# Kernel tuning notes

Measured on AMD Instinct MI355X. Metric: run time of the kernel, lower is better.

## Reference

```python
import jax, jax.numpy as jnp
import numpy as np
from jax import lax

INPLANES = 512
PLANES = 512
MID = PLANES // 4  # expansion = 4
G = 4              # patch_groups
EPS = 1e-5


def _conv(x, w, groups, pad):
    return lax.conv_general_dilated(
        x, w, window_strides=(1, 1), padding=[(pad, pad), (pad, pad)],
        dimension_numbers=('NCHW', 'OIHW', 'NCHW'), feature_group_count=groups)


def _bn(x, gamma, beta, mean, var):
    scale = gamma / jnp.sqrt(var + EPS)
    return x * scale[None, :, None, None] + (beta - mean * scale)[None, :, None, None]


def _upmask(mask, c, h, w):
    # [b,g,mh,mw] -> repeat each group over c//g channels (group-major channel order),
    # then nearest-upsample to (h, w) (exact integer repeat, matches F.interpolate nearest)
    b, g, mh, mw = mask.shape
    m = jnp.repeat(mask, c // g, axis=1)
    m = jnp.repeat(m, h // mh, axis=2)
    m = jnp.repeat(m, w // mw, axis=3)
    return m


def setup_inputs() -> dict:
    key = jax.random.key(0)
    ks = jax.random.split(key, 20)
    x = jax.random.normal(ks[0], (16, INPLANES, 56, 56), dtype=jnp.float32)
    mask = jax.random.randint(ks[1], (16, G, 7, 7), 0, 2).astype(jnp.float32)
    s = 0.05
    w1 = jax.random.normal(ks[2], (MID, INPLANES // G, 1, 1), dtype=jnp.float32) * s
    w2 = jax.random.normal(ks[3], (MID, MID // G, 3, 3), dtype=jnp.float32) * s
    w3 = jax.random.normal(ks[4], (PLANES, MID // G, 1, 1), dtype=jnp.float32) * s
    def bnp(k, c):
        k1, k2, k3, k4 = jax.random.split(k, 4)
        return (jax.random.normal(k1, (c,), jnp.float32) * 0.1 + 1.0,  # gamma
                jax.random.normal(k2, (c,), jnp.float32) * 0.1,        # beta
                jax.random.normal(k3, (c,), jnp.float32) * 0.1,        # running mean
                jax.random.uniform(k4, (c,), jnp.float32, 0.5, 1.5))   # running var
    g1, b1, m1, v1 = bnp(ks[5], MID)
    g2, b2, m2, v2 = bnp(ks[6], MID)
    g3, b3, m3, v3 = bnp(ks[7], PLANES)
    return dict(x=x, mask=mask, w1=w1, g1=g1, b1=b1, m1=m1, v1=v1,
                w2=w2, g2=g2, b2=b2, m2=m2, v2=v2,
                w3=w3, g3=g3, b3=b3, m3=m3, v3=v3)


def reference(x, mask, w1, g1, b1, m1, v1, w2, g2, b2, m2, v2, w3, g3, b3, m3, v3):
    b, c, h, w = x.shape
    residual = x
    mask1 = _upmask(mask, c, h, w)           # [b, c, h, w]
    out = x * mask1
    out = jax.nn.relu(_bn(_conv(out, w1, G, 0), g1, b1, m1, v1))  # [b, MID, h, w]
    mask2 = _upmask(mask, out.shape[1], h, w)
    out = out * mask2
    out = jax.nn.relu(_bn(_conv(out, w2, G, 1), g2, b2, m2, v2))
    out = out * mask2
    out = _bn(_conv(out, w3, G, 0), g3, b3, m3, v3)
    out = out + residual
    return jax.nn.relu(out)
```

## Files before the change

### kernel.cpp

```cpp
#include <hip/hip_runtime.h>
#include <stdint.h>

typedef unsigned short U16;
typedef unsigned int   U32;
typedef __attribute__((ext_vector_type(8))) short short8;
typedef __attribute__((ext_vector_type(4))) float floatx4;

#define HW 3136

__device__ __forceinline__ U16 f2b(float f){
    union { float f; unsigned int i; } v; v.f = f;
    unsigned int u = (v.i + 0x7FFFu + ((v.i >> 16) & 1u)) >> 16;
    return (U16)u;
}
__device__ __forceinline__ short8 pack8(const float* p){
    float4 a = *reinterpret_cast<const float4*>(p);
    float4 b = *reinterpret_cast<const float4*>(p + 4);
    short8 r;
    r[0]=(short)f2b(a.x); r[1]=(short)f2b(a.y); r[2]=(short)f2b(a.z); r[3]=(short)f2b(a.w);
    r[4]=(short)f2b(b.x); r[5]=(short)f2b(b.y); r[6]=(short)f2b(b.z); r[7]=(short)f2b(b.w);
    return r;
}

__global__ void k_pre(const float* __restrict__ w2,
                      const float* g1, const float* b1, const float* m1, const float* v1,
                      const float* g2, const float* b2, const float* m2, const float* v2,
                      const float* g3, const float* b3, const float* m3, const float* v3,
                      U16* __restrict__ w2t, float* __restrict__ bn){
  int i = blockIdx.x * 256 + threadIdx.x;
  if (i < 4*9*32*32) {
    int ic  = i & 31;
    int oc  = (i >> 5) & 31;
    int gt  = i >> 10;
    int g_  = gt / 9, tap = gt % 9;
    w2t[i] = f2b(w2[((g_*32 + oc)*32 + ic)*9 + tap]);
  } else {
    int j = i - 4*9*32*32;
    if (j >= 768) return;
    const float *gp, *bp, *mp, *vp; int c, so, sho;
    if (j < 128)      { c = j;       gp=g1; bp=b1; mp=m1; vp=v1; so = 0;   sho = 128;  }
    else if (j < 256) { c = j - 128; gp=g2; bp=b2; mp=m2; vp=v2; so = 256; sho = 384;  }
    else              { c = j - 256; gp=g3; bp=b3; mp=m3; vp=v3; so = 512; sho = 1024; }
    float s = gp[c] / sqrtf(vp[c] + 1e-5f);
    bn[so + c]  = s;
    bn[sho + c] = bp[c] - mp[c] * s;
  }
}

__global__ __launch_bounds__(512) void k_conv1(const float* __restrict__ x,
        const float* __restrict__ mask, const float* __restrict__ w1,
        const float* __restrict__ bn, U16* __restrict__ t1){
  const int t = threadIdx.x;
  const int lane = t & 63, wave = t >> 6;
  const int quad = lane >> 4, l15 = lane & 15;
  const int oct = wave & 1, pxq = wave >> 1;
  const int b = blockIdx.z, g = blockIdx.y, mh = blockIdx.x;
  const int h0 = mh*8, wbase = pxq*112;
  __shared__ float mk[7];
  __shared__ __align__(16) U16 xs[32*456];
  if (t < 7) mk[t] = mask[((b*4 + g)*7 + mh)*7 + t];
  const float* xg = x + (size_t)(b*512 + g*128)*HW + h0*56;
  U16* t1g = t1 + (size_t)(b*128 + g*32)*HW + h0*56;

  const float* wg = w1 + (size_t)(g*32)*128;
  short8 afr[4];
  #pragma unroll
  for (int ks = 0; ks < 4; ++ks)
    afr[ks] = pack8(wg + (oct*16 + l15)*128 + ks*32 + quad*8);

  floatx4 acc[7] = {};
  #pragma unroll
  for (int ch = 0; ch < 4; ++ch){
    __syncthreads();
    #pragma unroll
    for (int k = 0; k < 7; ++k){
      int idx = k*512 + t;
      int ic = idx / 112, f = idx - ic*112;
      int px = f*4;
      float4 v = *reinterpret_cast<const float4*>(xg + (size_t)(ch*32 + ic)*HW + px);
      float m = mk[(px % 56) >> 3];
      U32 lo = (U32)f2b(v.x*m) | ((U32)f2b(v.y*m) << 16);
      U32 hi = (U32)f2b(v.z*m) | ((U32)f2b(v.w*m) << 16);
      *reinterpret_cast<uint2*>(&xs[ic*456 + px]) = make_uint2(lo, hi);
    }
    __syncthreads();
    #pragma unroll
    for (int pxt = 0; pxt < 7; ++pxt){
      short8 bfr;
      #pragma unroll
      for (int j = 0; j < 8; ++j)
        bfr[j] = (short)xs[(quad*8 + j)*456 + wbase + pxt*16 + l15];
      acc[pxt] = __builtin_amdgcn_mfma_f32_16x16x32_bf16(afr[ch], bfr, acc[pxt], 0,0,0);
    }
  }
  #pragma unroll
  for (int reg = 0; reg < 4; ++reg){
    int oc = oct*16 + quad*4 + reg;
    float sc = bn[g*32 + oc], sh = bn[128 + g*32 + oc];
    #pragma unroll
    for (int pxt = 0; pxt < 7; ++pxt){
      int px = wbase + pxt*16 + l15;
      float y = fmaxf(sc*acc[pxt][reg] + sh, 0.0f) * mk[(px % 56) >> 3];
      t1g[(size_t)oc*HW + px] = f2b(y);
    }
  }
}

__global__ __launch_bounds__(512) void k_conv2(const U16* __restrict__ t1,
        const float* __restrict__ mask, const U16* __restrict__ w2t,
        const float* __restrict__ bn, U16* __restrict__ t2){
  const int t = threadIdx.x;
  const int lane = t & 63, wave = t >> 6;
  const int quad = lane >> 4, l15 = lane & 15;
  const int oct = wave & 1, rq = wave >> 1;
  const int b = blockIdx.z, g = blockIdx.y, mh = blockIdx.x;
  const int h0 = mh*8;
  __shared__ float mk[7];
  __shared__ __align__(16) U16 s[32*720];
  if (t < 7) mk[t] = mask[((b*4 + g)*7 + mh)*7 + t];
  if (t < 320){
    int ic = t / 10, r = t - ic*10;
    s[(ic*10 + r)*72 + 7]  = 0;
    s[(ic*10 + r)*72 + 64] = 0;
  }
  const U16* tg = t1 + (size_t)(b*128 + g*32)*HW;
  #pragma unroll
  for (int k = 0; k < 5; ++k){
    int idx = k*512 + t;
    if (idx < 2240){
      int ic = idx / 70, rem = idx - ic*70;
      int r = rem / 7, seg = rem - r*7;
      int hh = h0 - 1 + r;
      uint4 v = make_uint4(0,0,0,0);
      if (hh >= 0 && hh < 56)
        v = *reinterpret_cast<const uint4*>(tg + (size_t)ic*HW + hh*56 + seg*8);
      *reinterpret_cast<uint4*>(&s[(ic*10 + r)*72 + 8 + seg*8]) = v;
    }
  }
  __syncthreads();
  const U16* wg = w2t + g*9*32*32;
  floatx4 acc[7] = {};
  #pragma unroll
  for (int kh = 0; kh < 3; ++kh){
    const int lr = rq*2 + (l15 >> 3) + kh;
    #pragma unroll
    for (int kw = 0; kw < 3; ++kw){
      int tap = kh*3 + kw;
      short8 a0 = *reinterpret_cast<const short8*>(wg + (tap*32 + oct*16 + l15)*32 + quad*8);
      #pragma unroll
      for (int pxt = 0; pxt < 7; ++pxt){
        int lc = 7 + pxt*8 + (l15 & 7) + kw;
        short8 bfr;
        #pragma unroll
        for (int j = 0; j < 8; ++j)
          bfr[j] = (short)s[((quad*8 + j)*10 + lr)*72 + lc];
        acc[pxt] = __builtin_amdgcn_mfma_f32_16x16x32_bf16(a0, bfr, acc[pxt], 0,0,0);
      }
    }
  }
  U16* og = t2 + (size_t)(b*128 + g*32)*HW + h0*56;
  const int pr = rq*2 + (l15 >> 3);
  #pragma unroll
  for (int reg = 0; reg < 4; ++reg){
    int oc = oct*16 + quad*4 + reg;
    float sc = bn[256 + g*32 + oc], sh = bn[384 + g*32 + oc];
    #pragma unroll
    for (int pxt = 0; pxt < 7; ++pxt){
      float y = fmaxf(sc*acc[pxt][reg] + sh, 0.0f) * mk[pxt];
      og[oc*HW + pr*56 + pxt*8 + (l15 & 7)] = f2b(y);
    }
  }
}

__global__ __launch_bounds__(1024) void k_conv3(const U16* __restrict__ t2,
        const float* __restrict__ x, const float* __restrict__ w3,
        const float* __restrict__ bn, float* __restrict__ out){
  const int t = threadIdx.x;
  const int lane = t & 63, wave = t >> 6;
  const int quad = lane >> 4, l15 = lane & 15;
  const int pxq = wave & 3, ocp = wave >> 2;
  const int b = blockIdx.z, g = blockIdx.y, mh = blockIdx.x;
  const int h0 = mh*8, wbase = pxq*112;
  __shared__ __align__(16) U16 xs[32*456];
  const U16* tg = t2 + (size_t)(b*128 + g*32)*HW + h0*56;
  #pragma unroll
  for (int k = 0; k < 2; ++k){
    int idx = k*1024 + t;
    if (idx < 1792){
      int ic = idx / 56, seg = idx - ic*56;
      *reinterpret_cast<uint4*>(&xs[ic*456 + seg*8]) =
          *reinterpret_cast<const uint4*>(tg + (size_t)ic*HW + seg*8);
    }
  }
  __syncthreads();
  short8 bfr[7];
  #pragma unroll
  for (int pxt = 0; pxt < 7; ++pxt)
    #pragma unroll
    for (int j = 0; j < 8; ++j)
      bfr[pxt][j] = (short)xs[(quad*8 + j)*456 + wbase + pxt*16 + l15];
  const float* xg = x + (size_t)(b*512 + g*128)*HW + h0*56;
  float* og = out + (size_t)(b*512 + g*128)*HW + h0*56;
  #pragma unroll
  for (int o2 = 0; o2 < 2; ++o2){
    const int oct = ocp*2 + o2;
    short8 afr = pack8(w3 + (size_t)(g*128 + oct*16 + l15)*32 + quad*8);
    floatx4 acc[7] = {};
    #pragma unroll
    for (int pxt = 0; pxt < 7; ++pxt)
      acc[pxt] = __builtin_amdgcn_mfma_f32_16x16x32_bf16(afr, bfr[pxt], acc[pxt], 0,0,0);
    #pragma unroll
    for (int reg = 0; reg < 4; ++reg){
      int oc = oct*16 + quad*4 + reg;
      float sc = bn[512 + g*128 + oc], sh = bn[1024 + g*128 + oc];
      #pragma unroll
      for (int pxt = 0; pxt < 7; ++pxt){
        size_t o2i = (size_t)oc*HW + wbase + pxt*16 + l15;
        og[o2i] = fmaxf(sc*acc[pxt][reg] + sh + xg[o2i], 0.0f);
      }
    }
  }
}

extern "C" void kernel_launch(void* const* d_in, const int* in_sizes, int n_in,
                              void* d_out, int out_size, void* d_ws, size_t ws_size,
                              hipStream_t stream){
  const float* x    = (const float*)d_in[0];
  const float* mask = (const float*)d_in[1];
  const float* w1   = (const float*)d_in[2];
  const float* g1   = (const float*)d_in[3];
  const float* b1   = (const float*)d_in[4];
  const float* m1   = (const float*)d_in[5];
  const float* v1   = (const float*)d_in[6];
  const float* w2   = (const float*)d_in[7];
  const float* g2   = (const float*)d_in[8];
  const float* b2   = (const float*)d_in[9];
  const float* m2   = (const float*)d_in[10];
  const float* v2   = (const float*)d_in[11];
  const float* w3   = (const float*)d_in[12];
  const float* g3   = (const float*)d_in[13];
  const float* b3   = (const float*)d_in[14];
  const float* m3   = (const float*)d_in[15];
  const float* v3   = (const float*)d_in[16];

  char* ws = (char*)d_ws;
  U16*   w2t = (U16*)ws;
  float* bn  = (float*)(ws + 73728);
  U16*   t1  = (U16*)(ws + 79872);
  U16*   t2  = (U16*)(ws + 79872 + 12845056);

  k_pre<<<147, 256, 0, stream>>>(w2, g1,b1,m1,v1, g2,b2,m2,v2, g3,b3,m3,v3, w2t, bn);
  dim3 grid(7, 4, 16);
  k_conv1<<<grid, 512, 0, stream>>>(x, mask, w1, bn, t1);
  k_conv2<<<grid, 512, 0, stream>>>(t1, mask, w2t, bn, t2);
  k_conv3<<<grid, 1024, 0, stream>>>(t2, x, w3, bn, (float*)d_out);
}
```

Before: 270.7 us.

## Halve spatial tile to 4 rows per block, doubling grid for more parallelism

Each block now covers 4 image rows instead of 8, so the grid doubles from 448 to 896 blocks across all three conv kernels. Work per wave shrinks and pixel tiles are split unevenly (3 or 4 per wave), and conv2 now uses a flattened pixel-tile mapping with per-lane row/col indices and a 6-row halo. conv3 drops to 512 threads, with each wave owning one 16-channel output tile across 14 pixel tiles. The aim is better CU occupancy and load balance on a 256-CU part, at the cost of more halo reloading in conv2 and less register-level reuse.

```diff
diff --git a/kernel.cpp b/kernel.cpp
--- a/kernel.cpp
+++ b/kernel.cpp
@@ -51,14 +51,15 @@
         const float* __restrict__ mask, const float* __restrict__ w1,
         const float* __restrict__ bn, U16* __restrict__ t1){
   const int t = threadIdx.x;
-  const int lane = t & 63, wave = t >> 6;
+  const int lane = t & 63, w = t >> 6;
   const int quad = lane >> 4, l15 = lane & 15;
-  const int oct = wave & 1, pxq = wave >> 1;
-  const int b = blockIdx.z, g = blockIdx.y, mh = blockIdx.x;
-  const int h0 = mh*8, wbase = pxq*112;
+  const int oct = w & 1, pxq = w >> 1;
+  const int b = blockIdx.z, g = blockIdx.y, bx = blockIdx.x;
+  const int h0 = bx*4;
+  const int tt0 = (7*pxq) >> 1, tt1 = (7*(pxq+1)) >> 1;
   __shared__ float mk[7];
-  __shared__ __align__(16) U16 xs[32*456];
-  if (t < 7) mk[t] = mask[((b*4 + g)*7 + mh)*7 + t];
+  __shared__ __align__(16) U16 xs[32*228];
+  if (t < 7) mk[t] = mask[((b*4 + g)*7 + (h0>>3))*7 + t];
   const float* xg = x + (size_t)(b*512 + g*128)*HW + h0*56;
   U16* t1g = t1 + (size_t)(b*128 + g*32)*HW + h0*56;
 
@@ -68,29 +69,35 @@
   for (int ks = 0; ks < 4; ++ks)
     afr[ks] = pack8(wg + (oct*16 + l15)*128 + ks*32 + quad*8);
 
-  floatx4 acc[7] = {};
+  floatx4 acc[4] = {};
   #pragma unroll
   for (int ch = 0; ch < 4; ++ch){
     __syncthreads();
     #pragma unroll
-    for (int k = 0; k < 7; ++k){
+    for (int k = 0; k < 4; ++k){
       int idx = k*512 + t;
-      int ic = idx / 112, f = idx - ic*112;
-      int px = f*4;
-      float4 v = *reinterpret_cast<const float4*>(xg + (size_t)(ch*32 + ic)*HW + px);
-      float m = mk[(px % 56) >> 3];
-      U32 lo = (U32)f2b(v.x*m) | ((U32)f2b(v.y*m) << 16);
-      U32 hi = (U32)f2b(v.z*m) | ((U32)f2b(v.w*m) << 16);
-      *reinterpret_cast<uint2*>(&xs[ic*456 + px]) = make_uint2(lo, hi);
+      if (idx < 1792){
+        int ic = idx / 56, f = idx - ic*56;
+        int px = f*4;
+        int col = px % 56;
+        float4 v = *reinterpret_cast<const float4*>(xg + (size_t)(ch*32 + ic)*HW + px);
+        float m = mk[col >> 3];
+        U32 lo = (U32)f2b(v.x*m) | ((U32)f2b(v.y*m) << 16);
+        U32 hi = (U32)f2b(v.z*m) | ((U32)f2b(v.w*m) << 16);
+        *reinterpret_cast<uint2*>(&xs[ic*228 + px]) = make_uint2(lo, hi);
+      }
     }
     __syncthreads();
     #pragma unroll
-    for (int pxt = 0; pxt < 7; ++pxt){
-      short8 bfr;
-      #pragma unroll
-      for (int j = 0; j < 8; ++j)
-        bfr[j] = (short)xs[(quad*8 + j)*456 + wbase + pxt*16 + l15];
-      acc[pxt] = __builtin_amdgcn_mfma_f32_16x16x32_bf16(afr[ch], bfr, acc[pxt], 0,0,0);
+    for (int i = 0; i < 4; ++i){
+      int tt = tt0 + i;
+      if (tt < tt1){
+        short8 bfr;
+        #pragma unroll
+        for (int j = 0; j < 8; ++j)
+          bfr[j] = (short)xs[(quad*8 + j)*228 + tt*16 + l15];
+        acc[i] = __builtin_amdgcn_mfma_f32_16x16x32_bf16(afr[ch], bfr, acc[i], 0,0,0);
+      }
     }
   }
   #pragma unroll
@@ -98,10 +105,13 @@
     int oc = oct*16 + quad*4 + reg;
     float sc = bn[g*32 + oc], sh = bn[128 + g*32 + oc];
     #pragma unroll
-    for (int pxt = 0; pxt < 7; ++pxt){
-      int px = wbase + pxt*16 + l15;
-      float y = fmaxf(sc*acc[pxt][reg] + sh, 0.0f) * mk[(px % 56) >> 3];
-      t1g[(size_t)oc*HW + px] = f2b(y);
+    for (int i = 0; i < 4; ++i){
+      int tt = tt0 + i;
+      if (tt < tt1){
+        int px = tt*16 + l15;
+        float y = fmaxf(sc*acc[i][reg] + sh, 0.0f) * mk[(px % 56) >> 3];
+        t1g[(size_t)oc*HW + px] = f2b(y);
+      }
     }
   }
 }
@@ -110,114 +120,119 @@
         const float* __restrict__ mask, const U16* __restrict__ w2t,
         const float* __restrict__ bn, U16* __restrict__ t2){
   const int t = threadIdx.x;
-  const int lane = t & 63, wave = t >> 6;
+  const int lane = t & 63, w = t >> 6;
   const int quad = lane >> 4, l15 = lane & 15;
-  const int oct = wave & 1, rq = wave >> 1;
-  const int b = blockIdx.z, g = blockIdx.y, mh = blockIdx.x;
-  const int h0 = mh*8;
+  const int oct = w & 1, pxq = w >> 1;
+  const int b = blockIdx.z, g = blockIdx.y, bx = blockIdx.x;
+  const int h0 = bx*4;
+  const int tt0 = (7*pxq) >> 1, tt1 = (7*(pxq+1)) >> 1;
   __shared__ float mk[7];
-  __shared__ __align__(16) U16 s[32*720];
-  if (t < 7) mk[t] = mask[((b*4 + g)*7 + mh)*7 + t];
-  if (t < 320){
-    int ic = t / 10, r = t - ic*10;
-    s[(ic*10 + r)*72 + 7]  = 0;
-    s[(ic*10 + r)*72 + 64] = 0;
+  __shared__ __align__(16) U16 s[32*432];
+  if (t < 7) mk[t] = mask[((b*4 + g)*7 + (h0>>3))*7 + t];
+  if (t < 384){
+    int ic = t / 12, rr = (t % 12) >> 1;
+    s[(ic*6 + rr)*72 + ((t & 1) ? 64 : 7)] = 0;
   }
   const U16* tg = t1 + (size_t)(b*128 + g*32)*HW;
   #pragma unroll
-  for (int k = 0; k < 5; ++k){
+  for (int k = 0; k < 3; ++k){
     int idx = k*512 + t;
-    if (idx < 2240){
-      int ic = idx / 70, rem = idx - ic*70;
+    if (idx < 1344){
+      int ic = idx / 42, rem = idx - ic*42;
       int r = rem / 7, seg = rem - r*7;
       int hh = h0 - 1 + r;
       uint4 v = make_uint4(0,0,0,0);
       if (hh >= 0 && hh < 56)
         v = *reinterpret_cast<const uint4*>(tg + (size_t)ic*HW + hh*56 + seg*8);
-      *reinterpret_cast<uint4*>(&s[(ic*10 + r)*72 + 8 + seg*8]) = v;
+      *reinterpret_cast<uint4*>(&s[(ic*6 + r)*72 + 8 + seg*8]) = v;
     }
   }
   __syncthreads();
-  const U16* wg = w2t + g*9*32*32;
-  floatx4 acc[7] = {};
-  #pragma unroll
-  for (int kh = 0; kh < 3; ++kh){
-    const int lr = rq*2 + (l15 >> 3) + kh;
+  int rl[4], cl[4]; float mm[4];
+  #pragma unroll
+  for (int i = 0; i < 4; ++i){
+    int tt = tt0 + i;
+    if (tt < tt1){
+      int px = tt*16 + l15;
+      rl[i] = px / 56; cl[i] = px - rl[i]*56;
+      mm[i] = mk[cl[i] >> 3];
+    }
+  }
+  const U16* wg2 = w2t + g*9*32*32;
+  floatx4 acc[4] = {};
+  #pragma unroll
+  for (int kh = 0; kh < 3; ++kh)
     #pragma unroll
     for (int kw = 0; kw < 3; ++kw){
       int tap = kh*3 + kw;
-      short8 a0 = *reinterpret_cast<const short8*>(wg + (tap*32 + oct*16 + l15)*32 + quad*8);
+      short8 a0 = *reinterpret_cast<const short8*>(wg2 + (tap*32 + oct*16 + l15)*32 + quad*8);
       #pragma unroll
-      for (int pxt = 0; pxt < 7; ++pxt){
-        int lc = 7 + pxt*8 + (l15 & 7) + kw;
-        short8 bfr;
-        #pragma unroll
-        for (int j = 0; j < 8; ++j)
-          bfr[j] = (short)s[((quad*8 + j)*10 + lr)*72 + lc];
-        acc[pxt] = __builtin_amdgcn_mfma_f32_16x16x32_bf16(a0, bfr, acc[pxt], 0,0,0);
-      }
-    }
-  }
+      for (int i = 0; i < 4; ++i){
+        int tt = tt0 + i;
+        if (tt < tt1){
+          short8 bfr;
+          #pragma unroll
+          for (int j = 0; j < 8; ++j)
+            bfr[j] = (short)s[((quad*8 + j)*6 + rl[i] + kh)*72 + 7 + cl[i] + kw];
+          acc[i] = __builtin_amdgcn_mfma_f32_16x16x32_bf16(a0, bfr, acc[i], 0,0,0);
+        }
+      }
+    }
   U16* og = t2 + (size_t)(b*128 + g*32)*HW + h0*56;
-  const int pr = rq*2 + (l15 >> 3);
   #pragma unroll
   for (int reg = 0; reg < 4; ++reg){
     int oc = oct*16 + quad*4 + reg;
     float sc = bn[256 + g*32 + oc], sh = bn[384 + g*32 + oc];
     #pragma unroll
-    for (int pxt = 0; pxt < 7; ++pxt){
-      float y = fmaxf(sc*acc[pxt][reg] + sh, 0.0f) * mk[pxt];
-      og[oc*HW + pr*56 + pxt*8 + (l15 & 7)] = f2b(y);
-    }
-  }
-}
-
-__global__ __launch_bounds__(1024) void k_conv3(const U16* __restrict__ t2,
+    for (int i = 0; i < 4; ++i){
+      int tt = tt0 + i;
+      if (tt < tt1){
+        int px = tt*16 + l15;
+        float y = fmaxf(sc*acc[i][reg] + sh, 0.0f) * mm[i];
+        og[(size_t)oc*HW + px] = f2b(y);
+      }
+    }
+  }
+}
+
+__global__ __launch_bounds__(512) void k_conv3(const U16* __restrict__ t2,
         const float* __restrict__ x, const float* __restrict__ w3,
         const float* __restrict__ bn, float* __restrict__ out){
   const int t = threadIdx.x;
-  const int lane = t & 63, wave = t >> 6;
+  const int lane = t & 63, w = t >> 6;
   const int quad = lane >> 4, l15 = lane & 15;
-  const int pxq = wave & 3, ocp = wave >> 2;
-  const int b = blockIdx.z, g = blockIdx.y, mh = blockIdx.x;
-  const int h0 = mh*8, wbase = pxq*112;
-  __shared__ __align__(16) U16 xs[32*456];
+  const int b = blockIdx.z, g = blockIdx.y, bx = blockIdx.x;
+  const int h0 = bx*4;
+  __shared__ __align__(16) U16 xs[32*232];
   const U16* tg = t2 + (size_t)(b*128 + g*32)*HW + h0*56;
   #pragma unroll
   for (int k = 0; k < 2; ++k){
-    int idx = k*1024 + t;
-    if (idx < 1792){
-      int ic = idx / 56, seg = idx - ic*56;
-      *reinterpret_cast<uint4*>(&xs[ic*456 + seg*8]) =
+    int idx = k*512 + t;
+    if (idx < 896){
+      int ic = idx / 28, seg = idx - ic*28;
+      *reinterpret_cast<uint4*>(&xs[ic*232 + seg*8]) =
           *reinterpret_cast<const uint4*>(tg + (size_t)ic*HW + seg*8);
     }
   }
   __syncthreads();
-  short8 bfr[7];
-  #pragma unroll
-  for (int pxt = 0; pxt < 7; ++pxt)
-    #pragma unroll
-    for (int j = 0; j < 8; ++j)
-      bfr[pxt][j] = (short)xs[(quad*8 + j)*456 + wbase + pxt*16 + l15];
+  short8 afr = pack8(w3 + (size_t)(g*128 + w*16 + l15)*32 + quad*8);
+  const float* scp = bn + 512 + g*128 + w*16 + quad*4;
+  const float* shp = bn + 1024 + g*128 + w*16 + quad*4;
   const float* xg = x + (size_t)(b*512 + g*128)*HW + h0*56;
   float* og = out + (size_t)(b*512 + g*128)*HW + h0*56;
   #pragma unroll
-  for (int o2 = 0; o2 < 2; ++o2){
-    const int oct = ocp*2 + o2;
-    short8 afr = pack8(w3 + (size_t)(g*128 + oct*16 + l15)*32 + quad*8);
-    floatx4 acc[7] = {};
-    #pragma unroll
-    for (int pxt = 0; pxt < 7; ++pxt)
-      acc[pxt] = __builtin_amdgcn_mfma_f32_16x16x32_bf16(afr, bfr[pxt], acc[pxt], 0,0,0);
+  for (int tt = 0; tt < 14; ++tt){
+    short8 bfr;
+    #pragma unroll
+    for (int j = 0; j < 8; ++j)
+      bfr[j] = (short)xs[(quad*8 + j)*232 + tt*16 + l15];
+    floatx4 acc = {};
+    acc = __builtin_amdgcn_mfma_f32_16x16x32_bf16(afr, bfr, acc, 0,0,0);
+    int px = tt*16 + l15;
     #pragma unroll
     for (int reg = 0; reg < 4; ++reg){
-      int oc = oct*16 + quad*4 + reg;
-      float sc = bn[512 + g*128 + oc], sh = bn[1024 + g*128 + oc];
-      #pragma unroll
-      for (int pxt = 0; pxt < 7; ++pxt){
-        size_t o2i = (size_t)oc*HW + wbase + pxt*16 + l15;
-        og[o2i] = fmaxf(sc*acc[pxt][reg] + sh + xg[o2i], 0.0f);
-      }
+      size_t o2 = (size_t)(w*16 + quad*4 + reg)*HW + px;
+      og[o2] = fmaxf(scp[reg]*acc[reg] + shp[reg] + xg[o2], 0.0f);
     }
   }
 }
@@ -250,8 +265,8 @@
   U16*   t2  = (U16*)(ws + 79872 + 12845056);
 
   k_pre<<<147, 256, 0, stream>>>(w2, g1,b1,m1,v1, g2,b2,m2,v2, g3,b3,m3,v3, w2t, bn);
-  dim3 grid(7, 4, 16);
+  dim3 grid(14, 4, 16);
   k_conv1<<<grid, 512, 0, stream>>>(x, mask, w1, bn, t1);
   k_conv2<<<grid, 512, 0, stream>>>(t1, mask, w2t, bn, t2);
-  k_conv3<<<grid, 1024, 0, stream>>>(t2, x, w3, bn, (float*)d_out);
-}
+  k_conv3<<<grid, 512, 0, stream>>>(t2, x, w3, bn, (float*)d_out);
+}
```

Result: slower. 305.9 us (+13.0%).

## Fuse 3x3 conv2 and 1x1 conv3 into one kernel via shared-memory intermediate

Applied to the files above, without the earlier changes.

Merges the conv2 and conv3 kernels so the conv2 output tile stays in LDS instead of being written to and reread from a global bf16 buffer. Conv3 now runs in 8 waves of 512 threads, each wave owning 16 output channels and looping over 28 pixel tiles, instead of 16 waves over 1024 threads. This removes one launch and the t2 global round trip. In exchange the block uses more LDS, which may lower occupancy, and the conv3 phase has less per-block parallelism.

```diff
diff --git a/kernel.cpp b/kernel.cpp
--- a/kernel.cpp
+++ b/kernel.cpp
@@ -106,17 +106,18 @@
   }
 }
 
-__global__ __launch_bounds__(512) void k_conv2(const U16* __restrict__ t1,
+__global__ __launch_bounds__(512) void k_conv23(const U16* __restrict__ t1,
         const float* __restrict__ mask, const U16* __restrict__ w2t,
-        const float* __restrict__ bn, U16* __restrict__ t2){
+        const float* __restrict__ w3, const float* __restrict__ bn,
+        const float* __restrict__ x, float* __restrict__ out){
   const int t = threadIdx.x;
   const int lane = t & 63, wave = t >> 6;
   const int quad = lane >> 4, l15 = lane & 15;
-  const int oct = wave & 1, rq = wave >> 1;
   const int b = blockIdx.z, g = blockIdx.y, mh = blockIdx.x;
   const int h0 = mh*8;
   __shared__ float mk[7];
   __shared__ __align__(16) U16 s[32*720];
+  __shared__ __align__(16) U16 t2s[32*456];
   if (t < 7) mk[t] = mask[((b*4 + g)*7 + mh)*7 + t];
   if (t < 320){
     int ic = t / 10, r = t - ic*10;
@@ -138,85 +139,62 @@
     }
   }
   __syncthreads();
-  const U16* wg = w2t + g*9*32*32;
-  floatx4 acc[7] = {};
-  #pragma unroll
-  for (int kh = 0; kh < 3; ++kh){
-    const int lr = rq*2 + (l15 >> 3) + kh;
-    #pragma unroll
-    for (int kw = 0; kw < 3; ++kw){
-      int tap = kh*3 + kw;
-      short8 a0 = *reinterpret_cast<const short8*>(wg + (tap*32 + oct*16 + l15)*32 + quad*8);
-      #pragma unroll
-      for (int pxt = 0; pxt < 7; ++pxt){
-        int lc = 7 + pxt*8 + (l15 & 7) + kw;
-        short8 bfr;
+
+  {
+    const int oct = wave & 1, rq = wave >> 1;
+    const U16* wg = w2t + g*9*32*32;
+    floatx4 acc[7] = {};
+    #pragma unroll
+    for (int kh = 0; kh < 3; ++kh){
+      const int lr = rq*2 + (l15 >> 3) + kh;
+      #pragma unroll
+      for (int kw = 0; kw < 3; ++kw){
+        int tap = kh*3 + kw;
+        short8 a0 = *reinterpret_cast<const short8*>(wg + (tap*32 + oct*16 + l15)*32 + quad*8);
         #pragma unroll
-        for (int j = 0; j < 8; ++j)
-          bfr[j] = (short)s[((quad*8 + j)*10 + lr)*72 + lc];
-        acc[pxt] = __builtin_amdgcn_mfma_f32_16x16x32_bf16(a0, bfr, acc[pxt], 0,0,0);
+        for (int pxt = 0; pxt < 7; ++pxt){
+          int lc = 7 + pxt*8 + (l15 & 7) + kw;
+          short8 bfr;
+          #pragma unroll
+          for (int j = 0; j < 8; ++j)
+            bfr[j] = (short)s[((quad*8 + j)*10 + lr)*72 + lc];
+          acc[pxt] = __builtin_amdgcn_mfma_f32_16x16x32_bf16(a0, bfr, acc[pxt], 0,0,0);
+        }
       }
     }
-  }
-  U16* og = t2 + (size_t)(b*128 + g*32)*HW + h0*56;
-  const int pr = rq*2 + (l15 >> 3);
-  #pragma unroll
-  for (int reg = 0; reg < 4; ++reg){
-    int oc = oct*16 + quad*4 + reg;
-    float sc = bn[256 + g*32 + oc], sh = bn[384 + g*32 + oc];
-    #pragma unroll
-    for (int pxt = 0; pxt < 7; ++pxt){
-      float y = fmaxf(sc*acc[pxt][reg] + sh, 0.0f) * mk[pxt];
-      og[oc*HW + pr*56 + pxt*8 + (l15 & 7)] = f2b(y);
-    }
-  }
-}
-
-__global__ __launch_bounds__(1024) void k_conv3(const U16* __restrict__ t2,
-        const float* __restrict__ x, const float* __restrict__ w3,
-        const float* __restrict__ bn, float* __restrict__ out){
-  const int t = threadIdx.x;
-  const int lane = t & 63, wave = t >> 6;
-  const int quad = lane >> 4, l15 = lane & 15;
-  const int pxq = wave & 3, ocp = wave >> 2;
-  const int b = blockIdx.z, g = blockIdx.y, mh = blockIdx.x;
-  const int h0 = mh*8, wbase = pxq*112;
-  __shared__ __align__(16) U16 xs[32*456];
-  const U16* tg = t2 + (size_t)(b*128 + g*32)*HW + h0*56;
-  #pragma unroll
-  for (int k = 0; k < 2; ++k){
-    int idx = k*1024 + t;
-    if (idx < 1792){
-      int ic = idx / 56, seg = idx - ic*56;
-      *reinterpret_cast<uint4*>(&xs[ic*456 + seg*8]) =
-          *reinterpret_cast<const uint4*>(tg + (size_t)ic*HW + seg*8);
-    }
-  }
-  __syncthreads();
-  short8 bfr[7];
-  #pragma unroll
-  for (int pxt = 0; pxt < 7; ++pxt)
-    #pragma unroll
-    for (int j = 0; j < 8; ++j)
-      bfr[pxt][j] = (short)xs[(quad*8 + j)*456 + wbase + pxt*16 + l15];
-  const float* xg = x + (size_t)(b*512 + g*128)*HW + h0*56;
-  float* og = out + (size_t)(b*512 + g*128)*HW + h0*56;
-  #pragma unroll
-  for (int o2 = 0; o2 < 2; ++o2){
-    const int oct = ocp*2 + o2;
-    short8 afr = pack8(w3 + (size_t)(g*128 + oct*16 + l15)*32 + quad*8);
-    floatx4 acc[7] = {};
-    #pragma unroll
-    for (int pxt = 0; pxt < 7; ++pxt)
-      acc[pxt] = __builtin_amdgcn_mfma_f32_16x16x32_bf16(afr, bfr[pxt], acc[pxt], 0,0,0);
+    const int pr = rq*2 + (l15 >> 3);
     #pragma unroll
     for (int reg = 0; reg < 4; ++reg){
       int oc = oct*16 + quad*4 + reg;
-      float sc = bn[512 + g*128 + oc], sh = bn[1024 + g*128 + oc];
+      float sc = bn[256 + g*32 + oc], sh = bn[384 + g*32 + oc];
       #pragma unroll
       for (int pxt = 0; pxt < 7; ++pxt){
-        size_t o2i = (size_t)oc*HW + wbase + pxt*16 + l15;
-        og[o2i] = fmaxf(sc*acc[pxt][reg] + sh + xg[o2i], 0.0f);
+        float y = fmaxf(sc*acc[pxt][reg] + sh, 0.0f) * mk[pxt];
+        t2s[oc*456 + pr*56 + pxt*8 + (l15 & 7)] = f2b(y);
+      }
+    }
+  }
+  __syncthreads();
+
+  {
+    short8 afr = pack8(w3 + (size_t)(g*128 + wave*16 + l15)*32 + quad*8);
+    const float* scp = bn + 512 + g*128 + wave*16 + quad*4;
+    const float* shp = bn + 1024 + g*128 + wave*16 + quad*4;
+    const float* xg = x + (size_t)(b*512 + g*128)*HW + h0*56;
+    float* og = out + (size_t)(b*512 + g*128)*HW + h0*56;
+    #pragma unroll
+    for (int tt = 0; tt < 28; ++tt){
+      short8 bfr;
+      #pragma unroll
+      for (int j = 0; j < 8; ++j)
+        bfr[j] = (short)t2s[(quad*8 + j)*456 + tt*16 + l15];
+      floatx4 acc = {};
+      acc = __builtin_amdgcn_mfma_f32_16x16x32_bf16(afr, bfr, acc, 0,0,0);
+      int px = tt*16 + l15;
+      #pragma unroll
+      for (int reg = 0; reg < 4; ++reg){
+        size_t o2 = (size_t)(wave*16 + quad*4 + reg)*HW + px;
+        og[o2] = fmaxf(scp[reg]*acc[reg] + shp[reg] + xg[o2], 0.0f);
       }
     }
   }
@@ -247,11 +225,9 @@
   U16*   w2t = (U16*)ws;
   float* bn  = (float*)(ws + 73728);
   U16*   t1  = (U16*)(ws + 79872);
-  U16*   t2  = (U16*)(ws + 79872 + 12845056);
 
   k_pre<<<147, 256, 0, stream>>>(w2, g1,b1,m1,v1, g2,b2,m2,v2, g3,b3,m3,v3, w2t, bn);
   dim3 grid(7, 4, 16);
   k_conv1<<<grid, 512, 0, stream>>>(x, mask, w1, bn, t1);
-  k_conv2<<<grid, 512, 0, stream>>>(t1, mask, w2t, bn, t2);
-  k_conv3<<<grid, 1024, 0, stream>>>(t2, x, w3, bn, (float*)d_out);
-}
+  k_conv23<<<grid, 512, 0, stream>>>(t1, mask, w2t, w3, bn, x, (float*)d_out);
+}
```

New measurement: 287.0 us. 6.0% more time.
